# Performance work log

Measured on AMD Instinct MI355X. Metric: run time of the kernel, lower is better.

The kernel has to match this reference:

```python
import jax, jax.numpy as jnp
import numpy as np
from jax import lax

HID = 96              # hidden_dim (C)
DM  = 2 * HID         # SS2D d_model (real+imag interleaved channels)
DI  = 2 * DM          # d_inner (expand=2, VMamba default)
N   = 16              # d_state
K   = 4               # scan directions
R   = (DM + 15) // 16 # dt_rank = ceil(d_model/16)
B_, H_, W_ = 1, 64, 64


def _layernorm(x, w, b, eps=1e-5):
    m = x.mean(-1, keepdims=True)
    v = ((x - m) ** 2).mean(-1, keepdims=True)
    return (x - m) * lax.rsqrt(v + eps) * w + b


def _selective_scan(xs, delta, A, Bs, Cs):
    # xs, delta: (B,K,D,L); A: (K,D,N); Bs, Cs: (B,K,N,L)
    def step(h, inp):
        dt, Bt, Ct, ut = inp                              # (B,K,D),(B,K,N),(B,K,N),(B,K,D)
        dA = jnp.exp(dt[..., None] * A[None])             # (B,K,D,N)
        h = h * dA + dt[..., None] * Bt[:, :, None, :] * ut[..., None]
        y = jnp.einsum('bkdn,bkn->bkd', h, Ct)
        return h, y
    inputs = (jnp.moveaxis(delta, -1, 0), jnp.moveaxis(Bs, -1, 0),
              jnp.moveaxis(Cs, -1, 0), jnp.moveaxis(xs, -1, 0))
    h0 = jnp.zeros(xs.shape[:3] + (N,), xs.dtype)
    _, ys = lax.scan(step, h0, inputs)                    # (L,B,K,D)
    return jnp.moveaxis(ys, 0, -1)                        # (B,K,D,L)


def _forward_core(x, x_proj_w, dt_w, dt_b, A_logs, Ds):
    # x: (B, DI, H, W) -- 4-direction cross-scan (VMamba SS2D)
    B, D, H, W = x.shape
    L = H * W
    x_hw = x.reshape(B, D, L)
    x_wh = x.transpose(0, 1, 3, 2).reshape(B, D, L)
    x_hwwh = jnp.stack([x_hw, x_wh], axis=1)                    # (B,2,D,L)
    xs = jnp.concatenate([x_hwwh, jnp.flip(x_hwwh, -1)], 1)     # (B,4,D,L)
    x_dbl = jnp.einsum('bkdl,kcd->bkcl', xs, x_proj_w)          # (B,K,R+2N,L)
    dts, Bs, Cs = jnp.split(x_dbl, [R, R + N], axis=2)
    dts = jnp.einsum('bkrl,kdr->bkdl', dts, dt_w)
    delta = jax.nn.softplus(dts + dt_b[None, :, :, None])
    A = -jnp.exp(A_logs.reshape(K, D, N))
    ys = _selective_scan(xs, delta, A, Bs, Cs)
    out_y = ys + Ds.reshape(K, D)[None, :, :, None] * xs        # (B,4,D,L)
    inv_y = jnp.flip(out_y[:, 2:4], -1)
    tr = lambda t: t.reshape(B, D, W, H).transpose(0, 1, 3, 2).reshape(B, D, L)
    y = out_y[:, 0] + inv_y[:, 0] + tr(out_y[:, 1]) + tr(inv_y[:, 1])
    return y.transpose(0, 2, 1).reshape(B, H, W, D)


def _ss2d(x, in_proj_w, conv_w, conv_b, x_proj_w, dt_w, dt_b,
          A_logs, Ds, out_norm_w, out_norm_b, out_proj_w):
    # x: (B, H, Wf, DM)
    xz = x @ in_proj_w.T                                        # (B,H,Wf,2*DI)
    xc, z = jnp.split(xz, 2, axis=-1)
    xc = xc.transpose(0, 3, 1, 2)                               # (B,DI,H,Wf)
    xc = lax.conv_general_dilated(xc, conv_w, (1, 1), 'SAME',
                                  feature_group_count=DI,
                                  dimension_numbers=('NCHW', 'OIHW', 'NCHW'))
    xc = jax.nn.silu(xc + conv_b[None, :, None, None])
    y = _forward_core(xc, x_proj_w, dt_w, dt_b, A_logs, Ds)     # (B,H,Wf,DI)
    y = _layernorm(y, out_norm_w, out_norm_b)
    y = y * jax.nn.silu(z)
    return y @ out_proj_w.T                                     # (B,H,Wf,DM)


def _freq_vss(x, in_proj_w, conv_w, conv_b, x_proj_w, dt_w, dt_b,
              A_logs, Ds, out_norm_w, out_norm_b, out_proj_w):
    B, H, W, C = x.shape
    xf = jnp.fft.rfft2(x, axes=(1, 2), norm='ortho')            # (B,H,Wf,C) complex
    Wf = xf.shape[2]
    # interleave real/imag into channels: (B,H,Wf,C,2) -> (B,H,Wf,2C)
    x1 = jnp.stack([xf.real, xf.imag], axis=4).reshape(B, H, Wf, 2 * C)
    att = _ss2d(x1, in_proj_w, conv_w, conv_b, x_proj_w, dt_w, dt_b,
                A_logs, Ds, out_norm_w, out_norm_b, out_proj_w)
    att = att.reshape(B, H, Wf, C, 2)
    attc = lax.complex(att[..., 0], att[..., 1])
    x1r = jnp.fft.irfft2(attc, s=(H, W), axes=(1, 2), norm='ortho')
    return x + x1r                                              # residual (drop_path=0)


def setup_inputs() -> dict:
    key = jax.random.key(0)
    ks = jax.random.split(key, 8)
    s = 0.02
    return {
        'x': jax.random.normal(ks[0], (B_, H_, W_, HID), jnp.float32),
        'in_proj_w': jax.random.normal(ks[1], (2 * DI, DM), jnp.float32) * s,
        'conv_w': jax.random.normal(ks[2], (DI, 1, 3, 3), jnp.float32) * s,
        'conv_b': jnp.zeros((DI,), jnp.float32),
        'x_proj_w': jax.random.normal(ks[3], (K, R + 2 * N, DI), jnp.float32) * s,
        'dt_w': jax.random.normal(ks[4], (K, DI, R), jnp.float32) * s,
        'dt_b': jax.random.normal(ks[5], (K, DI), jnp.float32) * 0.1,
        'A_logs': jnp.tile(jnp.log(jnp.arange(1, N + 1, dtype=jnp.float32))[None], (K * DI, 1)),
        'Ds': jnp.ones((K * DI,), jnp.float32),
        'out_norm_w': jnp.ones((DI,), jnp.float32),
        'out_norm_b': jnp.zeros((DI,), jnp.float32),
        'out_proj_w': jax.random.normal(ks[6], (DM, DI), jnp.float32) * s,
    }


def reference(x, in_proj_w, conv_w, conv_b, x_proj_w, dt_w, dt_b,
              A_logs, Ds, out_norm_w, out_norm_b, out_proj_w):
    return _freq_vss(x, in_proj_w, conv_w, conv_b, x_proj_w, dt_w, dt_b,
                     A_logs, Ds, out_norm_w, out_norm_b, out_proj_w)
```

## Files before the change

kernel.cpp:

```cpp
#include <hip/hip_runtime.h>
#include <hip/hip_bf16.h>

#define LQ   2112
#define DQ   384
#define NST  16
#define HQ   64
#define WFQ  33
#define CQ   96
#define SC   66
#define KDN  24576

#define AIPW  0
#define ACW   147456
#define ACB   150912
#define AXPW  151296
#define ADTW  218880
#define ADTB  237312
#define AANEG 238848
#define ADS   263424
#define ANW   264960
#define ANB   265344
#define AOPW  265728
#define ARTOT 339456

#define ABIP     339456
#define BXP_OFF  147456
#define BOP_OFF  215040

#define OFF_FFT   483840
#define OFF_XZ    889344
#define OFF_XCV   2511360
#define OFF_XCVB  3322368
#define OFF_G     3727872
#define OFF_SUMDT 4099584
#define OFF_HEND  4200960
#define OFF_YS    5822976
#define OFF_YS4   6228480

typedef __attribute__((ext_vector_type(8))) __bf16 bf16x8;
typedef __attribute__((ext_vector_type(2))) __bf16 bf16x2;
typedef __attribute__((ext_vector_type(4))) float f32x4;

static __device__ __forceinline__ float u2f(unsigned short u)
{ union { unsigned int i; float f; } v; v.i = ((unsigned int)u) << 16; return v.f; }

static __device__ __forceinline__ float ldin(const void* p, int o, int isbf)
{
    if (isbf) return u2f(((const unsigned short*)p)[o]);
    return ((const float*)p)[o];
}

static __device__ __forceinline__ int isbf_of(const void* ds)
{ return (((const unsigned int*)ds)[0] == 0x3F803F80u) ? 1 : 0; }

__global__ __launch_bounds__(256) void k_cvt_rfftw(
    const void* __restrict__ x,   const void* __restrict__ ipw,
    const void* __restrict__ cw,  const void* __restrict__ cb,
    const void* __restrict__ xpw, const void* __restrict__ dtw,
    const void* __restrict__ dtb, const void* __restrict__ alog,
    const void* __restrict__ ds,  const void* __restrict__ nw,
    const void* __restrict__ nb,  const void* __restrict__ opw,
    float* __restrict__ arena, float2* __restrict__ Zc)
{
    const int isbf = isbf_of(ds);
    __bf16* bw = (__bf16*)(arena + ABIP);
    if (blockIdx.x < 1326) {
        int t = blockIdx.x * 256 + threadIdx.x;
        int o = t;
        if (o < 147456) { float v = ldin(ipw, o, isbf); arena[t] = v; bw[o] = (__bf16)v; return; }
        o -= 147456;
        if (o < 3456)   { arena[t] = ldin(cw, o, isbf);  return; }  o -= 3456;
        if (o < 384)    { arena[t] = ldin(cb, o, isbf);  return; }  o -= 384;
        if (o < 67584)  { float v = ldin(xpw, o, isbf); arena[t] = v; bw[BXP_OFF + o] = (__bf16)v; return; }
        o -= 67584;
        if (o < 18432)  { arena[t] = ldin(dtw, o, isbf); return; }  o -= 18432;
        if (o < 1536)   { arena[t] = ldin(dtb, o, isbf); return; }  o -= 1536;
        if (o < 24576)  { arena[t] = -expf(ldin(alog, o, isbf)); return; }  o -= 24576;
        if (o < 1536)   { arena[t] = ldin(ds, o, isbf);  return; }  o -= 1536;
        if (o < 384)    { arena[t] = ldin(nw, o, isbf);  return; }  o -= 384;
        if (o < 384)    { arena[t] = ldin(nb, o, isbf);  return; }  o -= 384;
        { float v = ldin(opw, o, isbf); arena[t] = v; bw[BOP_OFF + o] = (__bf16)v; }
        return;
    }
    __shared__ float tc[64], ts[64];
    if (threadIdx.x < 64) {
        float ang = -6.283185307179586f * (float)threadIdx.x / 64.f;
        float s, c; __sincosf(ang, &s, &c); tc[threadIdx.x] = c; ts[threadIdx.x] = s;
    }
    __syncthreads();
    int tid = (blockIdx.x - 1326) * 256 + threadIdx.x;
    int c = tid % CQ; int f = (tid / CQ) % WFQ; int h = tid / (CQ * WFQ);
    const int base = h * 64 * CQ + c;
    float zr = 0.f, zi = 0.f; int j = 0;
#pragma unroll 4
    for (int w = 0; w < 64; w++) {
        float xv = ldin(x, base + w * CQ, isbf);
        zr += xv * tc[j]; zi += xv * ts[j];
        j += f; j &= 63;
    }
    Zc[tid] = make_float2(zr, zi);
}

__global__ __launch_bounds__(256) void k_ffth(const float2* __restrict__ Zc, __bf16* __restrict__ x1b)
{
    __shared__ float tc[64], ts[64];
    if (threadIdx.x < 64) {
        float ang = -6.283185307179586f * (float)threadIdx.x / 64.f;
        float s, c; __sincosf(ang, &s, &c); tc[threadIdx.x] = c; ts[threadIdx.x] = s;
    }
    __syncthreads();
    int tid = blockIdx.x * 256 + threadIdx.x;
    int c = tid % CQ; int f = (tid / CQ) % WFQ; int u = tid / (CQ * WFQ);
    float xr = 0.f, xi = 0.f; int j = 0;
    int base = f * CQ + c;
#pragma unroll 4
    for (int h = 0; h < 64; h++) {
        float2 z = Zc[base + h * (WFQ * CQ)];
        xr += z.x * tc[j] - z.y * ts[j];
        xi += z.x * ts[j] + z.y * tc[j];
        j += u; j &= 63;
    }
    int l = u * WFQ + f;
    bf16x2 v = { (__bf16)(xr * (1.f / 64.f)), (__bf16)(xi * (1.f / 64.f)) };
    *(bf16x2*)(x1b + l * 192 + 2 * c) = v;
}

__global__ __launch_bounds__(256) void k_gemm(const __bf16* __restrict__ A, const __bf16* __restrict__ W,
                                              float* __restrict__ C, int N, int K)
{
    __shared__ __bf16 Asm[64 * 40];
    __shared__ __bf16 Bsm[64 * 40];
    const int tid = threadIdx.x;
    const int bm = blockIdx.y * 64, bn = blockIdx.x * 64;
    const int wv = tid >> 6, lane = tid & 63;
    const int srow = tid >> 2, skk = (tid & 3) * 8;
    const int fm = lane & 15, fq = lane >> 4;
    f32x4 acc0 = {0.f, 0.f, 0.f, 0.f}, acc1 = acc0, acc2 = acc0, acc3 = acc0;
    const __bf16* afp = Asm + (wv * 16 + fm) * 40 + fq * 8;
    const __bf16* bfp = Bsm + fm * 40 + fq * 8;
    for (int k0 = 0; k0 < K; k0 += 32) {
        *(bf16x8*)(Asm + srow * 40 + skk) =
            *(const bf16x8*)(A + (size_t)(bm + srow) * K + k0 + skk);
        {
            bf16x8 v = { (__bf16)0.f, (__bf16)0.f, (__bf16)0.f, (__bf16)0.f,
                         (__bf16)0.f, (__bf16)0.f, (__bf16)0.f, (__bf16)0.f };
            if (bn + srow < N)
                v = *(const bf16x8*)(W + (size_t)(bn + srow) * K + k0 + skk);
            *(bf16x8*)(Bsm + srow * 40 + skk) = v;
        }
        __syncthreads();
        bf16x8 af = *(const bf16x8*)afp;
        bf16x8 fb0 = *(const bf16x8*)(bfp);
        bf16x8 fb1 = *(const bf16x8*)(bfp + 16 * 40);
        bf16x8 fb2 = *(const bf16x8*)(bfp + 32 * 40);
        bf16x8 fb3 = *(const bf16x8*)(bfp + 48 * 40);
        acc0 = __builtin_amdgcn_mfma_f32_16x16x32_bf16(af, fb0, acc0, 0, 0, 0);
        acc1 = __builtin_amdgcn_mfma_f32_16x16x32_bf16(af, fb1, acc1, 0, 0, 0);
        acc2 = __builtin_amdgcn_mfma_f32_16x16x32_bf16(af, fb2, acc2, 0, 0, 0);
        acc3 = __builtin_amdgcn_mfma_f32_16x16x32_bf16(af, fb3, acc3, 0, 0, 0);
        __syncthreads();
    }
    const int m0 = bm + wv * 16 + fq * 4;
#pragma unroll
    for (int nt = 0; nt < 4; nt++) {
        f32x4 a = (nt == 0) ? acc0 : ((nt == 1) ? acc1 : ((nt == 2) ? acc2 : acc3));
        int n = bn + nt * 16 + fm;
        if (n < N) {
#pragma unroll
            for (int r = 0; r < 4; r++)
                C[(size_t)(m0 + r) * N + n] = a[r];
        }
    }
}

__global__ __launch_bounds__(256) void k_conv(const float* __restrict__ xz,
                                              const float* __restrict__ ar,
                                              float* __restrict__ xcv, __bf16* __restrict__ xcvb)
{
    int tid = blockIdx.x * 256 + threadIdx.x;
    int d = tid % DQ; int lp = tid / DQ;
    int l0 = lp * 2;
    float w9[9];
#pragma unroll
    for (int i = 0; i < 9; i++) w9[i] = ar[ACW + d * 9 + i];
    float cb = ar[ACB + d];
#pragma unroll
    for (int q = 0; q < 2; q++) {
        int l = l0 + q;
        int h = l / WFQ; int f = l % WFQ;
        float acc = cb;
#pragma unroll
        for (int ky = 0; ky < 3; ky++) {
            int hh = h + ky - 1;
            if (hh < 0 || hh >= HQ) continue;
#pragma unroll
            for (int kx = 0; kx < 3; kx++) {
                int ff = f + kx - 1;
                if (ff < 0 || ff >= WFQ) continue;
                acc += w9[ky * 3 + kx] * xz[(size_t)(hh * WFQ + ff) * 768 + d];
            }
        }
        float sig = 1.f / (1.f + __expf(-acc));
        float val = acc * sig;
        xcv[(size_t)l * DQ + d] = val;
        xcvb[(size_t)l * DQ + d] = (__bf16)val;
    }
}

static __device__ __forceinline__ float softplus_f(float a)
{
    return (a > 15.f) ? a : __logf(1.f + __expf(a));
}

template<int KK> static __device__ __forceinline__ int chunk_l0(int s)
{
    if (KK == 0) return s * 32;
    if (KK == 1) return (s & 1) * 1056 + (s >> 1);
    if (KK == 2) return 2111 - s * 32;
    return 2111 - (s & 1) * 1056 - (s >> 1);
}
template<int KK> static __device__ __forceinline__ int chunk_stp()
{
    if (KK == 0) return 1;
    if (KK == 1) return 33;
    if (KK == 2) return -1;
    return -33;
}

template<int KK, int PASS2> static __device__ __forceinline__ void scan_body(
    const float* __restrict__ xcv, const float* __restrict__ G, const float* __restrict__ ar,
    float* __restrict__ hend, float* __restrict__ sumdt, float* __restrict__ ys4)
{
    const int s = blockIdx.x, db = blockIdx.y;
    const int lane = threadIdx.x;
    const int stp = chunk_stp<KK>();
    const int l0 = chunk_l0<KK>(s);
    const int kd = KK * DQ + db * 64 + lane;

    const float* wp = ar + ADTW + kd * 12;
    const float4 wA = *(const float4*)(wp);
    const float4 wB = *(const float4*)(wp + 4);
    const float4 wC = *(const float4*)(wp + 8);
    const float bias = ar[ADTB + kd];
    const float* ap = ar + AANEG + kd * 16;
    const float4 Av0 = *(const float4*)(ap);
    const float4 Av1 = *(const float4*)(ap + 4);
    const float4 Av2 = *(const float4*)(ap + 8);
    const float4 Av3 = *(const float4*)(ap + 12);

    float4 h0 = make_float4(0.f, 0.f, 0.f, 0.f), h1 = h0, h2 = h0, h3 = h0;
    if (PASS2) {
        const float* hp = hend + (size_t)s * KDN + kd * 16;
        h0 = *(const float4*)(hp);
        h1 = *(const float4*)(hp + 4);
        h2 = *(const float4*)(hp + 8);
        h3 = *(const float4*)(hp + 12);
    }

    float* ysk = ys4 + (size_t)KK * (LQ * DQ);
    float sd_acc = 0.f;
    for (int i = 0; i < 32; i++) {
        const int lt = l0 + stp * i;
        const float* gr = G + (size_t)lt * 176 + KK * 44;
        float4 g0 = *(const float4*)(gr);
        float4 g1 = *(const float4*)(gr + 4);
        float4 g2 = *(const float4*)(gr + 8);
        float u = xcv[(size_t)lt * DQ + db * 64 + lane];
        float acc = bias
            + wA.x * g0.x + wA.y * g0.y + wA.z * g0.z + wA.w * g0.w
            + wB.x * g1.x + wB.y * g1.y + wB.z * g1.z + wB.w * g1.w
            + wC.x * g2.x + wC.y * g2.y + wC.z * g2.z + wC.w * g2.w;
        float dt = softplus_f(acc);
        float du = dt * u;
        float4 b0 = *(const float4*)(gr + 12);
        float4 b1 = *(const float4*)(gr + 16);
        float4 b2 = *(const float4*)(gr + 20);
        float4 b3 = *(const float4*)(gr + 24);
        h0.x = h0.x * __expf(dt * Av0.x) + du * b0.x;
        h0.y = h0.y * __expf(dt * Av0.y) + du * b0.y;
        h0.z = h0.z * __expf(dt * Av0.z) + du * b0.z;
        h0.w = h0.w * __expf(dt * Av0.w) + du * b0.w;
        h1.x = h1.x * __expf(dt * Av1.x) + du * b1.x;
        h1.y = h1.y * __expf(dt * Av1.y) + du * b1.y;
        h1.z = h1.z * __expf(dt * Av1.z) + du * b1.z;
        h1.w = h1.w * __expf(dt * Av1.w) + du * b1.w;
        h2.x = h2.x * __expf(dt * Av2.x) + du * b2.x;
        h2.y = h2.y * __expf(dt * Av2.y) + du * b2.y;
        h2.z = h2.z * __expf(dt * Av2.z) + du * b2.z;
        h2.w = h2.w * __expf(dt * Av2.w) + du * b2.w;
        h3.x = h3.x * __expf(dt * Av3.x) + du * b3.x;
        h3.y = h3.y * __expf(dt * Av3.y) + du * b3.y;
        h3.z = h3.z * __expf(dt * Av3.z) + du * b3.z;
        h3.w = h3.w * __expf(dt * Av3.w) + du * b3.w;
        if (PASS2) {
            float4 c0 = *(const float4*)(gr + 28);
            float4 c1 = *(const float4*)(gr + 32);
            float4 c2 = *(const float4*)(gr + 36);
            float4 c3 = *(const float4*)(gr + 40);
            float y0 = h0.x * c0.x + h0.y * c0.y + h0.z * c0.z + h0.w * c0.w;
            float y1 = h1.x * c1.x + h1.y * c1.y + h1.z * c1.z + h1.w * c1.w;
            float y2 = h2.x * c2.x + h2.y * c2.y + h2.z * c2.z + h2.w * c2.w;
            float y3 = h3.x * c3.x + h3.y * c3.y + h3.z * c3.z + h3.w * c3.w;
            ysk[(size_t)lt * DQ + db * 64 + lane] = (y0 + y1) + (y2 + y3);
        } else {
            sd_acc += dt;
        }
    }

    if (!PASS2) {
        float* hp = hend + (size_t)s * KDN + kd * 16;
        *(float4*)(hp)      = h0;
        *(float4*)(hp + 4)  = h1;
        *(float4*)(hp + 8)  = h2;
        *(float4*)(hp + 12) = h3;
        sumdt[s * 1536 + kd] = sd_acc;
    }
}

__global__ __launch_bounds__(64) void k_scan1(const float* __restrict__ xcv, const float* __restrict__ G,
                                              const float* __restrict__ ar,
                                              float* __restrict__ hend, float* __restrict__ sumdt,
                                              float* __restrict__ ys4)
{
    switch (blockIdx.z) {
        case 0: scan_body<0, 0>(xcv, G, ar, hend, sumdt, ys4); break;
        case 1: scan_body<1, 0>(xcv, G, ar, hend, sumdt, ys4); break;
        case 2: scan_body<2, 0>(xcv, G, ar, hend, sumdt, ys4); break;
        default: scan_body<3, 0>(xcv, G, ar, hend, sumdt, ys4); break;
    }
}

__global__ __launch_bounds__(64) void k_scan2(const float* __restrict__ xcv, const float* __restrict__ G,
                                              const float* __restrict__ ar,
                                              float* __restrict__ hend, float* __restrict__ sumdt,
                                              float* __restrict__ ys4)
{
    switch (blockIdx.z) {
        case 0: scan_body<0, 1>(xcv, G, ar, hend, sumdt, ys4); break;
        case 1: scan_body<1, 1>(xcv, G, ar, hend, sumdt, ys4); break;
        case 2: scan_body<2, 1>(xcv, G, ar, hend, sumdt, ys4); break;
        default: scan_body<3, 1>(xcv, G, ar, hend, sumdt, ys4); break;
    }
}

__global__ __launch_bounds__(256) void k_comb(const float* __restrict__ ar, const float* __restrict__ sumdt,
                                              float* __restrict__ hend)
{
    int tid = blockIdx.x * 256 + threadIdx.x;
    int kd = tid >> 4;
    float Av = ar[AANEG + tid];
    float hbuf[6], sbuf[6];
#pragma unroll
    for (int q = 0; q < 6; q++) {
        hbuf[q] = hend[(size_t)q * KDN + tid];
        sbuf[q] = sumdt[q * 1536 + kd];
    }
    float hp = 0.f;
    for (int s = 0; s < SC; s += 6) {
        float hc[6], sc6[6];
#pragma unroll
        for (int q = 0; q < 6; q++) { hc[q] = hbuf[q]; sc6[q] = sbuf[q]; }
#pragma unroll
        for (int q = 0; q < 6; q++) {
            int sn = s + 6 + q;
            if (sn < SC) {
                hbuf[q] = hend[(size_t)sn * KDN + tid];
                sbuf[q] = sumdt[sn * 1536 + kd];
            }
        }
#pragma unroll
        for (int q = 0; q < 6; q++) {
            hend[(size_t)(s + q) * KDN + tid] = hp;
            hp = hp * __expf(Av * sc6[q]) + hc[q];
        }
    }
}

__global__ __launch_bounds__(128) void k_lnmul(const float* __restrict__ ys4, const float* __restrict__ xcv,
                                               const float* __restrict__ xz, const float* __restrict__ ar,
                                               __bf16* __restrict__ ymb)
{
    int l = blockIdx.x; int tid = threadIdx.x;
    float v[3]; float s1 = 0.f, s2 = 0.f;
#pragma unroll
    for (int j = 0; j < 3; j++) {
        int d = tid + j * 128;
        size_t idx = (size_t)l * DQ + d;
        float sd = ar[ADS + d] + ar[ADS + DQ + d] + ar[ADS + 2 * DQ + d] + ar[ADS + 3 * DQ + d];
        float a = ys4[idx] + ys4[811008 + idx] + ys4[1622016 + idx] + ys4[2433024 + idx]
                + sd * xcv[idx];
        v[j] = a; s1 += a; s2 += a * a;
    }
#pragma unroll
    for (int off = 1; off < 64; off <<= 1) { s1 += __shfl_xor(s1, off); s2 += __shfl_xor(s2, off); }
    __shared__ float sh[4];
    if ((tid & 63) == 0) { sh[(tid >> 6) * 2] = s1; sh[(tid >> 6) * 2 + 1] = s2; }
    __syncthreads();
    s1 = sh[0] + sh[2]; s2 = sh[1] + sh[3];
    float m = s1 * (1.f / 384.f);
    float var = s2 * (1.f / 384.f) - m * m;
    float rs = rsqrtf(var + 1e-5f);
#pragma unroll
    for (int j = 0; j < 3; j++) {
        int d = tid + j * 128;
        float z = xz[(size_t)l * 768 + 384 + d];
        float sig = 1.f / (1.f + __expf(-z));
        ymb[(size_t)l * DQ + d] = (__bf16)(((v[j] - m) * rs * ar[ANW + d] + ar[ANB + d]) * (z * sig));
    }
}

__global__ __launch_bounds__(256) void k_iffth(const float* __restrict__ att, float2* __restrict__ Yc)
{
    __shared__ float tc[64], ts[64];
    if (threadIdx.x < 64) {
        float ang = 6.283185307179586f * (float)threadIdx.x / 64.f;
        float s, c; __sincosf(ang, &s, &c); tc[threadIdx.x] = c; ts[threadIdx.x] = s;
    }
    __syncthreads();
    int tid = blockIdx.x * 256 + threadIdx.x;
    int c = tid % CQ; int f = (tid / CQ) % WFQ; int hp = tid / (CQ * WFQ);
    float yr = 0.f, yi = 0.f; int j = 0;
#pragma unroll 4
    for (int h = 0; h < 64; h++) {
        const float* ap = att + (size_t)(h * WFQ + f) * 192 + 2 * c;
        float arv = ap[0], aiv = ap[1];
        yr += arv * tc[j] - aiv * ts[j];
        yi += arv * ts[j] + aiv * tc[j];
        j += hp; j &= 63;
    }
    Yc[tid] = make_float2(yr * 0.125f, yi * 0.125f);
}

__global__ __launch_bounds__(256) void k_irfft_res(const float2* __restrict__ Yc,
                                                   const void* __restrict__ x, const void* __restrict__ ds,
                                                   void* __restrict__ out)
{
    __shared__ float tc[64], ts[64];
    if (threadIdx.x < 64) {
        float ang = 6.283185307179586f * (float)threadIdx.x / 64.f;
        float s, c; __sincosf(ang, &s, &c); tc[threadIdx.x] = c; ts[threadIdx.x] = s;
    }
    __syncthreads();
    const int isbf = isbf_of(ds);
    int tid = blockIdx.x * 256 + threadIdx.x;
    int c = tid % CQ; int w = (tid / CQ) % 64; int h = tid / (CQ * 64);
    const float2* yc = Yc + h * (WFQ * CQ) + c;
    float2 y0 = yc[0];
    float acc = y0.x;
    acc += ((w & 1) ? -1.f : 1.f) * yc[32 * CQ].x;
    float a2 = 0.f; int j = w & 63;
#pragma unroll 4
    for (int f = 1; f < 32; f++) {
        float2 yf = yc[f * CQ];
        a2 += yf.x * tc[j] - yf.y * ts[j];
        j += w; j &= 63;
    }
    acc += 2.f * a2;
    float val = ldin(x, tid, isbf) + 0.125f * acc;
    if (isbf) ((__hip_bfloat16*)out)[tid] = __float2bfloat16(val);
    else      ((float*)out)[tid] = val;
}

extern "C" void kernel_launch(void* const* d_in, const int* in_sizes, int n_in,
                              void* d_out, int out_size, void* d_ws, size_t ws_size,
                              hipStream_t stream)
{
    float* ws    = (float*)d_ws;
    float* ar    = ws;
    __bf16* bw   = (__bf16*)(ws + ABIP);
    float2* Zc   = (float2*)(ws + OFF_FFT);
    float* xz    = ws + OFF_XZ;
    float* xcv   = ws + OFF_XCV;
    __bf16* xcvb = (__bf16*)(ws + OFF_XCVB);
    float* G     = ws + OFF_G;
    float* sumdt = ws + OFF_SUMDT;
    float* hend  = ws + OFF_HEND;
    __bf16* x1b  = (__bf16*)(ws + OFF_YS);
    float* ys4   = ws + OFF_YS4;

    __bf16* ymb = (__bf16*)hend;
    float* att  = xcv;
    float2* Yc  = Zc;

    k_cvt_rfftw<<<2118, 256, 0, stream>>>(d_in[0], d_in[1], d_in[2], d_in[3], d_in[4], d_in[5],
                                          d_in[6], d_in[7], d_in[8], d_in[9], d_in[10], d_in[11],
                                          ar, Zc);
    k_ffth<<<792, 256, 0, stream>>>(Zc, x1b);
    k_gemm<<<dim3(12, 33), 256, 0, stream>>>(x1b, bw, xz, 768, 192);
    k_conv<<<1584, 256, 0, stream>>>(xz, ar, xcv, xcvb);
    k_gemm<<<dim3(3, 33), 256, 0, stream>>>(xcvb, bw + BXP_OFF, G, 176, 384);
    k_scan1<<<dim3(SC, 6, 4), 64, 0, stream>>>(xcv, G, ar, hend, sumdt, ys4);
    k_comb<<<96, 256, 0, stream>>>(ar, sumdt, hend);
    k_scan2<<<dim3(SC, 6, 4), 64, 0, stream>>>(xcv, G, ar, hend, sumdt, ys4);
    k_lnmul<<<LQ, 128, 0, stream>>>(ys4, xcv, xz, ar, ymb);
    k_gemm<<<dim3(3, 33), 256, 0, stream>>>(ymb, bw + BOP_OFF, att, 192, 384);
    k_iffth<<<792, 256, 0, stream>>>(att, Yc);
    k_irfft_res<<<1536, 256, 0, stream>>>(Yc, d_in[0], d_in[8], d_out);
}
```

Measured before the change: 202.0 us.

## Fuse 2D FFT and inverse FFT passes into per-channel shared-memory kernels

```diff
diff --git a/kernel.cpp b/kernel.cpp
--- a/kernel.cpp
+++ b/kernel.cpp
@@ -27,7 +27,6 @@
 #define BXP_OFF  147456
 #define BOP_OFF  215040
 
-#define OFF_FFT   483840
 #define OFF_XZ    889344
 #define OFF_XCV   2511360
 #define OFF_XCVB  3322368
@@ -53,14 +52,14 @@
 static __device__ __forceinline__ int isbf_of(const void* ds)
 { return (((const unsigned int*)ds)[0] == 0x3F803F80u) ? 1 : 0; }
 
-__global__ __launch_bounds__(256) void k_cvt_rfftw(
+__global__ __launch_bounds__(256) void k_fft2(
     const void* __restrict__ x,   const void* __restrict__ ipw,
     const void* __restrict__ cw,  const void* __restrict__ cb,
     const void* __restrict__ xpw, const void* __restrict__ dtw,
     const void* __restrict__ dtb, const void* __restrict__ alog,
     const void* __restrict__ ds,  const void* __restrict__ nw,
     const void* __restrict__ nb,  const void* __restrict__ opw,
-    float* __restrict__ arena, float2* __restrict__ Zc)
+    float* __restrict__ arena, __bf16* __restrict__ x1b)
 {
     const int isbf = isbf_of(ds);
     __bf16* bw = (__bf16*)(arena + ABIP);
@@ -82,47 +81,44 @@
         { float v = ldin(opw, o, isbf); arena[t] = v; bw[BOP_OFF + o] = (__bf16)v; }
         return;
     }
+    __shared__ float xpl[4096];
+    __shared__ float Zr[2112], Zi[2112];
     __shared__ float tc[64], ts[64];
-    if (threadIdx.x < 64) {
-        float ang = -6.283185307179586f * (float)threadIdx.x / 64.f;
-        float s, c; __sincosf(ang, &s, &c); tc[threadIdx.x] = c; ts[threadIdx.x] = s;
-    }
+    const int tid = threadIdx.x;
+    const int c = blockIdx.x - 1326;
+    if (tid < 64) {
+        float ang = -6.283185307179586f * (float)tid / 64.f;
+        float s, cc; __sincosf(ang, &s, &cc); tc[tid] = cc; ts[tid] = s;
+    }
+    for (int idx = tid; idx < 4096; idx += 256)
+        xpl[idx] = ldin(x, idx * 96 + c, isbf);
     __syncthreads();
-    int tid = (blockIdx.x - 1326) * 256 + threadIdx.x;
-    int c = tid % CQ; int f = (tid / CQ) % WFQ; int h = tid / (CQ * WFQ);
-    const int base = h * 64 * CQ + c;
-    float zr = 0.f, zi = 0.f; int j = 0;
+    for (int idx = tid; idx < 2112; idx += 256) {
+        int h = idx / 33, f = idx % 33;
+        const float* xr = xpl + h * 64;
+        float sr = 0.f, si = 0.f; int j = 0;
 #pragma unroll 4
-    for (int w = 0; w < 64; w++) {
-        float xv = ldin(x, base + w * CQ, isbf);
-        zr += xv * tc[j]; zi += xv * ts[j];
-        j += f; j &= 63;
-    }
-    Zc[tid] = make_float2(zr, zi);
-}
-
-__global__ __launch_bounds__(256) void k_ffth(const float2* __restrict__ Zc, __bf16* __restrict__ x1b)
-{
-    __shared__ float tc[64], ts[64];
-    if (threadIdx.x < 64) {
-        float ang = -6.283185307179586f * (float)threadIdx.x / 64.f;
-        float s, c; __sincosf(ang, &s, &c); tc[threadIdx.x] = c; ts[threadIdx.x] = s;
+        for (int w = 0; w < 64; w++) {
+            float xv = xr[w];
+            sr += xv * tc[j]; si += xv * ts[j];
+            j += f; j &= 63;
+        }
+        Zr[idx] = sr; Zi[idx] = si;
     }
     __syncthreads();
-    int tid = blockIdx.x * 256 + threadIdx.x;
-    int c = tid % CQ; int f = (tid / CQ) % WFQ; int u = tid / (CQ * WFQ);
-    float xr = 0.f, xi = 0.f; int j = 0;
-    int base = f * CQ + c;
+    for (int idx = tid; idx < 2112; idx += 256) {
+        int u = idx / 33, f = idx % 33;
+        float xr = 0.f, xi = 0.f; int j = 0;
 #pragma unroll 4
-    for (int h = 0; h < 64; h++) {
-        float2 z = Zc[base + h * (WFQ * CQ)];
-        xr += z.x * tc[j] - z.y * ts[j];
-        xi += z.x * ts[j] + z.y * tc[j];
-        j += u; j &= 63;
-    }
-    int l = u * WFQ + f;
-    bf16x2 v = { (__bf16)(xr * (1.f / 64.f)), (__bf16)(xi * (1.f / 64.f)) };
-    *(bf16x2*)(x1b + l * 192 + 2 * c) = v;
+        for (int h = 0; h < 64; h++) {
+            float zr = Zr[h * 33 + f], zi = Zi[h * 33 + f];
+            xr += zr * tc[j] - zi * ts[j];
+            xi += zr * ts[j] + zi * tc[j];
+            j += u; j &= 63;
+        }
+        bf16x2 v = { (__bf16)(xr * (1.f / 64.f)), (__bf16)(xi * (1.f / 64.f)) };
+        *(bf16x2*)(x1b + (size_t)idx * 192 + 2 * c) = v;
+    }
 }
 
 __global__ __launch_bounds__(256) void k_gemm(const __bf16* __restrict__ A, const __bf16* __restrict__ W,
@@ -409,56 +405,57 @@
     }
 }
 
-__global__ __launch_bounds__(256) void k_iffth(const float* __restrict__ att, float2* __restrict__ Yc)
-{
+__global__ __launch_bounds__(256) void k_ifft2(const float* __restrict__ att,
+                                               const void* __restrict__ x, const void* __restrict__ ds,
+                                               void* __restrict__ out)
+{
+    __shared__ float Ar[2112], Ai[2112];
+    __shared__ float Yr[2112], Yi[2112];
     __shared__ float tc[64], ts[64];
-    if (threadIdx.x < 64) {
-        float ang = 6.283185307179586f * (float)threadIdx.x / 64.f;
-        float s, c; __sincosf(ang, &s, &c); tc[threadIdx.x] = c; ts[threadIdx.x] = s;
+    const int tid = threadIdx.x;
+    const int c = blockIdx.x;
+    const int isbf = isbf_of(ds);
+    if (tid < 64) {
+        float ang = 6.283185307179586f * (float)tid / 64.f;
+        float s, cc; __sincosf(ang, &s, &cc); tc[tid] = cc; ts[tid] = s;
+    }
+    for (int idx = tid; idx < 2112; idx += 256) {
+        const float* ap = att + (size_t)idx * 192 + 2 * c;
+        Ar[idx] = ap[0]; Ai[idx] = ap[1];
     }
     __syncthreads();
-    int tid = blockIdx.x * 256 + threadIdx.x;
-    int c = tid % CQ; int f = (tid / CQ) % WFQ; int hp = tid / (CQ * WFQ);
-    float yr = 0.f, yi = 0.f; int j = 0;
+    for (int idx = tid; idx < 2112; idx += 256) {
+        int hp = idx / 33, f = idx % 33;
+        float yr = 0.f, yi = 0.f; int j = 0;
 #pragma unroll 4
-    for (int h = 0; h < 64; h++) {
-        const float* ap = att + (size_t)(h * WFQ + f) * 192 + 2 * c;
-        float arv = ap[0], aiv = ap[1];
-        yr += arv * tc[j] - aiv * ts[j];
-        yi += arv * ts[j] + aiv * tc[j];
-        j += hp; j &= 63;
-    }
-    Yc[tid] = make_float2(yr * 0.125f, yi * 0.125f);
-}
-
-__global__ __launch_bounds__(256) void k_irfft_res(const float2* __restrict__ Yc,
-                                                   const void* __restrict__ x, const void* __restrict__ ds,
-                                                   void* __restrict__ out)
-{
-    __shared__ float tc[64], ts[64];
-    if (threadIdx.x < 64) {
-        float ang = 6.283185307179586f * (float)threadIdx.x / 64.f;
-        float s, c; __sincosf(ang, &s, &c); tc[threadIdx.x] = c; ts[threadIdx.x] = s;
+        for (int h = 0; h < 64; h++) {
+            float arv = Ar[h * 33 + f], aiv = Ai[h * 33 + f];
+            yr += arv * tc[j] - aiv * ts[j];
+            yi += arv * ts[j] + aiv * tc[j];
+            j += hp; j &= 63;
+        }
+        Yr[idx] = yr * 0.125f;
+        Yi[idx] = yi * 0.125f;
     }
     __syncthreads();
-    const int isbf = isbf_of(ds);
-    int tid = blockIdx.x * 256 + threadIdx.x;
-    int c = tid % CQ; int w = (tid / CQ) % 64; int h = tid / (CQ * 64);
-    const float2* yc = Yc + h * (WFQ * CQ) + c;
-    float2 y0 = yc[0];
-    float acc = y0.x;
-    acc += ((w & 1) ? -1.f : 1.f) * yc[32 * CQ].x;
-    float a2 = 0.f; int j = w & 63;
+    for (int idx = tid; idx < 4096; idx += 256) {
+        int h = idx / 64, w = idx % 64;
+        const float* yrow_r = Yr + h * 33;
+        const float* yrow_i = Yi + h * 33;
+        float acc = yrow_r[0];
+        acc += ((w & 1) ? -1.f : 1.f) * yrow_r[32];
+        float a2 = 0.f; int j = w & 63;
 #pragma unroll 4
-    for (int f = 1; f < 32; f++) {
-        float2 yf = yc[f * CQ];
-        a2 += yf.x * tc[j] - yf.y * ts[j];
-        j += w; j &= 63;
-    }
-    acc += 2.f * a2;
-    float val = ldin(x, tid, isbf) + 0.125f * acc;
-    if (isbf) ((__hip_bfloat16*)out)[tid] = __float2bfloat16(val);
-    else      ((float*)out)[tid] = val;
+        for (int f = 1; f < 32; f++) {
+            a2 += yrow_r[f] * tc[j] - yrow_i[f] * ts[j];
+            j += w; j &= 63;
+        }
+        acc += 2.f * a2;
+        int gi = idx * 96 + c;
+        float val = ldin(x, gi, isbf) + 0.125f * acc;
+        if (isbf) ((__hip_bfloat16*)out)[gi] = __float2bfloat16(val);
+        else      ((float*)out)[gi] = val;
+    }
 }
 
 extern "C" void kernel_launch(void* const* d_in, const int* in_sizes, int n_in,
@@ -468,7 +465,6 @@
     float* ws    = (float*)d_ws;
     float* ar    = ws;
     __bf16* bw   = (__bf16*)(ws + ABIP);
-    float2* Zc   = (float2*)(ws + OFF_FFT);
     float* xz    = ws + OFF_XZ;
     float* xcv   = ws + OFF_XCV;
     __bf16* xcvb = (__bf16*)(ws + OFF_XCVB);
@@ -480,12 +476,10 @@
 
     __bf16* ymb = (__bf16*)hend;
     float* att  = xcv;
-    float2* Yc  = Zc;
-
-    k_cvt_rfftw<<<2118, 256, 0, stream>>>(d_in[0], d_in[1], d_in[2], d_in[3], d_in[4], d_in[5],
-                                          d_in[6], d_in[7], d_in[8], d_in[9], d_in[10], d_in[11],
-                                          ar, Zc);
-    k_ffth<<<792, 256, 0, stream>>>(Zc, x1b);
+
+    k_fft2<<<1422, 256, 0, stream>>>(d_in[0], d_in[1], d_in[2], d_in[3], d_in[4], d_in[5],
+                                     d_in[6], d_in[7], d_in[8], d_in[9], d_in[10], d_in[11],
+                                     ar, x1b);
     k_gemm<<<dim3(12, 33), 256, 0, stream>>>(x1b, bw, xz, 768, 192);
     k_conv<<<1584, 256, 0, stream>>>(xz, ar, xcv, xcvb);
     k_gemm<<<dim3(3, 33), 256, 0, stream>>>(xcvb, bw + BXP_OFF, G, 176, 384);
@@ -494,6 +488,5 @@
     k_scan2<<<dim3(SC, 6, 4), 64, 0, stream>>>(xcv, G, ar, hend, sumdt, ys4);
     k_lnmul<<<LQ, 128, 0, stream>>>(ys4, xcv, xz, ar, ymb);
     k_gemm<<<dim3(3, 33), 256, 0, stream>>>(ymb, bw + BOP_OFF, att, 192, 384);
-    k_iffth<<<792, 256, 0, stream>>>(att, Yc);
-    k_irfft_res<<<1536, 256, 0, stream>>>(Yc, d_in[0], d_in[8], d_out);
-}
+    k_ifft2<<<96, 256, 0, stream>>>(att, d_in[0], d_in[8], d_out);
+}
```

Measured after the change: 262.4 us. 29.9% more time.

## Fuse chunked scan passes and carry combine into one per-direction kernel

Applied to the files above, without the earlier changes.

```diff
diff --git a/kernel.cpp b/kernel.cpp
--- a/kernel.cpp
+++ b/kernel.cpp
@@ -32,7 +32,6 @@
 #define OFF_XCV   2511360
 #define OFF_XCVB  3322368
 #define OFF_G     3727872
-#define OFF_SUMDT 4099584
 #define OFF_HEND  4200960
 #define OFF_YS    5822976
 #define OFF_YS4   6228480
@@ -227,12 +226,11 @@
     return -33;
 }
 
-template<int KK, int PASS2> static __device__ __forceinline__ void scan_body(
+template<int KK, int PASS2> static __device__ __forceinline__ void scan_chunk(
+    int s, int db, int lane,
     const float* __restrict__ xcv, const float* __restrict__ G, const float* __restrict__ ar,
-    float* __restrict__ hend, float* __restrict__ sumdt, float* __restrict__ ys4)
-{
-    const int s = blockIdx.x, db = blockIdx.y;
-    const int lane = threadIdx.x;
+    float* __restrict__ hend, float* __restrict__ sumdtL, float* __restrict__ ys4)
+{
     const int stp = chunk_stp<KK>();
     const int l0 = chunk_l0<KK>(s);
     const int kd = KK * DQ + db * 64 + lane;
@@ -313,66 +311,65 @@
         *(float4*)(hp + 4)  = h1;
         *(float4*)(hp + 8)  = h2;
         *(float4*)(hp + 12) = h3;
-        sumdt[s * 1536 + kd] = sd_acc;
-    }
-}
-
-__global__ __launch_bounds__(64) void k_scan1(const float* __restrict__ xcv, const float* __restrict__ G,
-                                              const float* __restrict__ ar,
-                                              float* __restrict__ hend, float* __restrict__ sumdt,
-                                              float* __restrict__ ys4)
-{
-    switch (blockIdx.z) {
-        case 0: scan_body<0, 0>(xcv, G, ar, hend, sumdt, ys4); break;
-        case 1: scan_body<1, 0>(xcv, G, ar, hend, sumdt, ys4); break;
-        case 2: scan_body<2, 0>(xcv, G, ar, hend, sumdt, ys4); break;
-        default: scan_body<3, 0>(xcv, G, ar, hend, sumdt, ys4); break;
-    }
-}
-
-__global__ __launch_bounds__(64) void k_scan2(const float* __restrict__ xcv, const float* __restrict__ G,
-                                              const float* __restrict__ ar,
-                                              float* __restrict__ hend, float* __restrict__ sumdt,
-                                              float* __restrict__ ys4)
-{
-    switch (blockIdx.z) {
-        case 0: scan_body<0, 1>(xcv, G, ar, hend, sumdt, ys4); break;
-        case 1: scan_body<1, 1>(xcv, G, ar, hend, sumdt, ys4); break;
-        case 2: scan_body<2, 1>(xcv, G, ar, hend, sumdt, ys4); break;
-        default: scan_body<3, 1>(xcv, G, ar, hend, sumdt, ys4); break;
-    }
-}
-
-__global__ __launch_bounds__(256) void k_comb(const float* __restrict__ ar, const float* __restrict__ sumdt,
-                                              float* __restrict__ hend)
-{
-    int tid = blockIdx.x * 256 + threadIdx.x;
-    int kd = tid >> 4;
-    float Av = ar[AANEG + tid];
-    float hbuf[6], sbuf[6];
-#pragma unroll
-    for (int q = 0; q < 6; q++) {
-        hbuf[q] = hend[(size_t)q * KDN + tid];
-        sbuf[q] = sumdt[q * 1536 + kd];
-    }
-    float hp = 0.f;
-    for (int s = 0; s < SC; s += 6) {
-        float hc[6], sc6[6];
-#pragma unroll
-        for (int q = 0; q < 6; q++) { hc[q] = hbuf[q]; sc6[q] = sbuf[q]; }
-#pragma unroll
-        for (int q = 0; q < 6; q++) {
-            int sn = s + 6 + q;
-            if (sn < SC) {
-                hbuf[q] = hend[(size_t)sn * KDN + tid];
-                sbuf[q] = sumdt[sn * 1536 + kd];
+        sumdtL[s * 64 + lane] = sd_acc;
+    }
+}
+
+template<int KK> static __device__ __forceinline__ void scanall_body(
+    const float* __restrict__ xcv, const float* __restrict__ G, const float* __restrict__ ar,
+    float* __restrict__ hend, float* __restrict__ ys4, float* __restrict__ sumdtL)
+{
+    const int db = blockIdx.x;
+    const int wid = threadIdx.x >> 6, lane = threadIdx.x & 63;
+
+    for (int s = wid; s < SC; s += 16)
+        scan_chunk<KK, 0>(s, db, lane, xcv, G, ar, hend, sumdtL, ys4);
+    __syncthreads();
+
+    {
+        const int t = threadIdx.x;
+        const int dloc = t >> 4;
+        const int kd = KK * DQ + db * 64 + dloc;
+        const size_t idx = (size_t)kd * 16 + (t & 15);
+        const float Av = ar[AANEG + idx];
+        float hbuf[6];
+#pragma unroll
+        for (int q = 0; q < 6; q++) hbuf[q] = hend[(size_t)q * KDN + idx];
+        float hp = 0.f;
+        for (int s0 = 0; s0 < SC; s0 += 6) {
+            float hc[6];
+#pragma unroll
+            for (int q = 0; q < 6; q++) hc[q] = hbuf[q];
+#pragma unroll
+            for (int q = 0; q < 6; q++) {
+                int sn = s0 + 6 + q;
+                if (sn < SC) hbuf[q] = hend[(size_t)sn * KDN + idx];
+            }
+#pragma unroll
+            for (int q = 0; q < 6; q++) {
+                hend[(size_t)(s0 + q) * KDN + idx] = hp;
+                hp = hp * __expf(Av * sumdtL[(s0 + q) * 64 + dloc]) + hc[q];
             }
         }
-#pragma unroll
-        for (int q = 0; q < 6; q++) {
-            hend[(size_t)(s + q) * KDN + tid] = hp;
-            hp = hp * __expf(Av * sc6[q]) + hc[q];
-        }
+    }
+    __syncthreads();
+
+    for (int s = wid; s < SC; s += 16)
+        scan_chunk<KK, 1>(s, db, lane, xcv, G, ar, hend, sumdtL, ys4);
+}
+
+__global__ __launch_bounds__(1024, 1) void k_scanall(const float* __restrict__ xcv,
+                                                     const float* __restrict__ G,
+                                                     const float* __restrict__ ar,
+                                                     float* __restrict__ hend,
+                                                     float* __restrict__ ys4)
+{
+    __shared__ float sumdtL[SC * 64];
+    switch (blockIdx.y) {
+        case 0: scanall_body<0>(xcv, G, ar, hend, ys4, sumdtL); break;
+        case 1: scanall_body<1>(xcv, G, ar, hend, ys4, sumdtL); break;
+        case 2: scanall_body<2>(xcv, G, ar, hend, ys4, sumdtL); break;
+        default: scanall_body<3>(xcv, G, ar, hend, ys4, sumdtL); break;
     }
 }
 
@@ -473,7 +470,6 @@
     float* xcv   = ws + OFF_XCV;
     __bf16* xcvb = (__bf16*)(ws + OFF_XCVB);
     float* G     = ws + OFF_G;
-    float* sumdt = ws + OFF_SUMDT;
     float* hend  = ws + OFF_HEND;
     __bf16* x1b  = (__bf16*)(ws + OFF_YS);
     float* ys4   = ws + OFF_YS4;
@@ -489,9 +485,7 @@
     k_gemm<<<dim3(12, 33), 256, 0, stream>>>(x1b, bw, xz, 768, 192);
     k_conv<<<1584, 256, 0, stream>>>(xz, ar, xcv, xcvb);
     k_gemm<<<dim3(3, 33), 256, 0, stream>>>(xcvb, bw + BXP_OFF, G, 176, 384);
-    k_scan1<<<dim3(SC, 6, 4), 64, 0, stream>>>(xcv, G, ar, hend, sumdt, ys4);
-    k_comb<<<96, 256, 0, stream>>>(ar, sumdt, hend);
-    k_scan2<<<dim3(SC, 6, 4), 64, 0, stream>>>(xcv, G, ar, hend, sumdt, ys4);
+    k_scanall<<<dim3(6, 4), 1024, 0, stream>>>(xcv, G, ar, hend, ys4);
     k_lnmul<<<LQ, 128, 0, stream>>>(ys4, xcv, xz, ar, ymb);
     k_gemm<<<dim3(3, 33), 256, 0, stream>>>(ymb, bw + BOP_OFF, att, 192, 384);
     k_iffth<<<792, 256, 0, stream>>>(att, Yc);
```

New measurement: 484.3 us. +139.8%, slower.

## Fuse inverse column DFT and inverse row rFFT with residual into one kernel

Applied to the files above, without the earlier changes.

```diff
diff --git a/kernel.cpp b/kernel.cpp
--- a/kernel.cpp
+++ b/kernel.cpp
@@ -259,6 +259,7 @@
 
     float* ysk = ys4 + (size_t)KK * (LQ * DQ);
     float sd_acc = 0.f;
+#pragma unroll 2
     for (int i = 0; i < 32; i++) {
         const int lt = l0 + stp * i;
         const float* gr = G + (size_t)lt * 176 + KK * 44;
@@ -409,56 +410,60 @@
     }
 }
 
-__global__ __launch_bounds__(256) void k_iffth(const float* __restrict__ att, float2* __restrict__ Yc)
-{
+__global__ __launch_bounds__(256) void k_ifft2b(const float* __restrict__ att,
+                                                const void* __restrict__ x, const void* __restrict__ ds,
+                                                void* __restrict__ out)
+{
+    __shared__ float Ar[2112], Ai[2112];
+    __shared__ float Yr[528], Yi[528];
     __shared__ float tc[64], ts[64];
-    if (threadIdx.x < 64) {
-        float ang = 6.283185307179586f * (float)threadIdx.x / 64.f;
-        float s, c; __sincosf(ang, &s, &c); tc[threadIdx.x] = c; ts[threadIdx.x] = s;
+    const int tid = threadIdx.x;
+    const int c = blockIdx.x;
+    const int hg = blockIdx.y;
+    const int isbf = isbf_of(ds);
+    if (tid < 64) {
+        float ang = 6.283185307179586f * (float)tid / 64.f;
+        float s, cc; __sincosf(ang, &s, &cc); tc[tid] = cc; ts[tid] = s;
+    }
+    for (int idx = tid; idx < 2112; idx += 256) {
+        const float* ap = att + (size_t)idx * 192 + 2 * c;
+        Ar[idx] = ap[0]; Ai[idx] = ap[1];
     }
     __syncthreads();
-    int tid = blockIdx.x * 256 + threadIdx.x;
-    int c = tid % CQ; int f = (tid / CQ) % WFQ; int hp = tid / (CQ * WFQ);
-    float yr = 0.f, yi = 0.f; int j = 0;
+    for (int idx = tid; idx < 528; idx += 256) {
+        int hploc = idx / 33, f = idx % 33;
+        int hp = hg * 16 + hploc;
+        float yr = 0.f, yi = 0.f; int j = 0;
 #pragma unroll 4
-    for (int h = 0; h < 64; h++) {
-        const float* ap = att + (size_t)(h * WFQ + f) * 192 + 2 * c;
-        float arv = ap[0], aiv = ap[1];
-        yr += arv * tc[j] - aiv * ts[j];
-        yi += arv * ts[j] + aiv * tc[j];
-        j += hp; j &= 63;
-    }
-    Yc[tid] = make_float2(yr * 0.125f, yi * 0.125f);
-}
-
-__global__ __launch_bounds__(256) void k_irfft_res(const float2* __restrict__ Yc,
-                                                   const void* __restrict__ x, const void* __restrict__ ds,
-                                                   void* __restrict__ out)
-{
-    __shared__ float tc[64], ts[64];
-    if (threadIdx.x < 64) {
-        float ang = 6.283185307179586f * (float)threadIdx.x / 64.f;
-        float s, c; __sincosf(ang, &s, &c); tc[threadIdx.x] = c; ts[threadIdx.x] = s;
+        for (int h = 0; h < 64; h++) {
+            float arv = Ar[h * 33 + f], aiv = Ai[h * 33 + f];
+            yr += arv * tc[j] - aiv * ts[j];
+            yi += arv * ts[j] + aiv * tc[j];
+            j += hp; j &= 63;
+        }
+        Yr[idx] = yr * 0.125f;
+        Yi[idx] = yi * 0.125f;
     }
     __syncthreads();
-    const int isbf = isbf_of(ds);
-    int tid = blockIdx.x * 256 + threadIdx.x;
-    int c = tid % CQ; int w = (tid / CQ) % 64; int h = tid / (CQ * 64);
-    const float2* yc = Yc + h * (WFQ * CQ) + c;
-    float2 y0 = yc[0];
-    float acc = y0.x;
-    acc += ((w & 1) ? -1.f : 1.f) * yc[32 * CQ].x;
-    float a2 = 0.f; int j = w & 63;
+    for (int idx = tid; idx < 1024; idx += 256) {
+        int hloc = idx >> 6, w = idx & 63;
+        const float* yrr = Yr + hloc * 33;
+        const float* yri = Yi + hloc * 33;
+        float acc = yrr[0];
+        acc += ((w & 1) ? -1.f : 1.f) * yrr[32];
+        float a2 = 0.f; int j = w & 63;
 #pragma unroll 4
-    for (int f = 1; f < 32; f++) {
-        float2 yf = yc[f * CQ];
-        a2 += yf.x * tc[j] - yf.y * ts[j];
-        j += w; j &= 63;
-    }
-    acc += 2.f * a2;
-    float val = ldin(x, tid, isbf) + 0.125f * acc;
-    if (isbf) ((__hip_bfloat16*)out)[tid] = __float2bfloat16(val);
-    else      ((float*)out)[tid] = val;
+        for (int f = 1; f < 32; f++) {
+            a2 += yrr[f] * tc[j] - yri[f] * ts[j];
+            j += w; j &= 63;
+        }
+        acc += 2.f * a2;
+        int h = hg * 16 + hloc;
+        int gi = (h * 64 + w) * 96 + c;
+        float val = ldin(x, gi, isbf) + 0.125f * acc;
+        if (isbf) ((__hip_bfloat16*)out)[gi] = __float2bfloat16(val);
+        else      ((float*)out)[gi] = val;
+    }
 }
 
 extern "C" void kernel_launch(void* const* d_in, const int* in_sizes, int n_in,
@@ -480,7 +485,6 @@
 
     __bf16* ymb = (__bf16*)hend;
     float* att  = xcv;
-    float2* Yc  = Zc;
 
     k_cvt_rfftw<<<2118, 256, 0, stream>>>(d_in[0], d_in[1], d_in[2], d_in[3], d_in[4], d_in[5],
                                           d_in[6], d_in[7], d_in[8], d_in[9], d_in[10], d_in[11],
@@ -494,6 +498,5 @@
     k_scan2<<<dim3(SC, 6, 4), 64, 0, stream>>>(xcv, G, ar, hend, sumdt, ys4);
     k_lnmul<<<LQ, 128, 0, stream>>>(ys4, xcv, xz, ar, ymb);
     k_gemm<<<dim3(3, 33), 256, 0, stream>>>(ymb, bw + BOP_OFF, att, 192, 384);
-    k_iffth<<<792, 256, 0, stream>>>(att, Yc);
-    k_irfft_res<<<1536, 256, 0, stream>>>(Yc, d_in[0], d_in[8], d_out);
-}
+    k_ifft2b<<<dim3(96, 4), 256, 0, stream>>>(att, d_in[0], d_in[8], d_out);
+}
```

Result: slower. 208.0 us (+3.0%).
